# Optimization experiments

Hardware: AMD Instinct MI355X
Metric: run time of the kernel (lower is better)

Reference implementation:

```python
import jax, jax.numpy as jnp
import numpy as np

EPS = 1e-5
B, F, C, H, L, S = 8192, 128, 256, 512, 4, 10


def _gelu(x):
    return jax.nn.gelu(x, approximate=False)  # torch nn.GELU default = exact erf


def _ln(x, g, b):
    m = jnp.mean(x, axis=-1, keepdims=True)
    v = jnp.var(x, axis=-1, keepdims=True)  # biased, matches torch LayerNorm
    return (x - m) / jnp.sqrt(v + EPS) * g + b


def setup_inputs() -> dict:
    key = jax.random.key(0)
    ks = iter(jax.random.split(key, 40))

    def w(shape, fan_in):
        return jax.random.normal(next(ks), shape, jnp.float32) / np.float32(np.sqrt(fan_in))

    def z0(*s):
        return jnp.zeros(s, jnp.float32)

    return dict(
        x=jax.random.normal(next(ks), (B, F), jnp.float32),
        context=jax.random.normal(next(ks), (B, C), jnp.float32),
        u=jax.random.normal(next(ks), (S, B, F), jnp.float32),
        Wi=w((F, H), F), bi=z0(H),
        Wt1=w((1, H), 1), bt1=z0(H), Wt2=w((H, H), H), bt2=z0(H),
        Wc1=w((C, 2 * H), C), bc1=z0(2 * H), Wc2=w((2 * H, H), 2 * H), bc2=z0(H),
        Wv=w((L, H, H), H), bv=z0(L, H), Woa=w((L, H, H), H), boa=z0(L, H),
        g1=jnp.ones((L, H), jnp.float32), be1=z0(L, H),
        Wm1=w((L, H, 4 * H), H), bm1=z0(L, 4 * H),
        Wm2=w((L, 4 * H, H), 4 * H), bm2=z0(L, H),
        g2=jnp.ones((L, H), jnp.float32), be2=z0(L, H),
        Wcv=w((L, H, H), H), bcv=z0(L, H), Wco=w((L, H, H), H), bco=z0(L, H),
        scale=0.5 * jnp.ones((L,), jnp.float32),
        Wp1=w((H, H), H), bp1=z0(H), Wp2=w((H, F), H), bp2=z0(F),
    )


def _forward(x, context, u, Wi, bi, Wt1, bt1, Wt2, bt2, Wc1, bc1, Wc2, bc2,
             Wv, bv, Woa, boa, g1, be1, Wm1, bm1, Wm2, bm2, g2, be2,
             Wcv, bcv, Wco, bco, scale, Wp1, bp1, Wp2, bp2):
    n_steps = u.shape[0]
    dt = 1.0 / n_steps
    nb = x.shape[0]
    nl = Wv.shape[0]

    # context projection, computed once as in torch
    ctx = _gelu(context @ Wc1 + bc1) @ Wc2 + bc2  # [B,H]
    # seq_len==1 cross-attention: softmax over a single key == 1, so the output
    # is out_proj(v_proj(ctx)) and does not depend on x -> precompute per layer.
    vctx = jnp.einsum('bh,lhk->lbk', ctx, Wcv) + bcv[:, None, :]    # [L,B,H]
    xatt = jnp.einsum('lbh,lhk->lbk', vctx, Wco) + bco[:, None, :]  # [L,B,H]

    def vel(z, t):
        tt = jnp.clip(t, 0.0, 1.0)[:, None]                          # [B,1]
        h = z @ Wi + bi + (_gelu(tt @ Wt1 + bt1) @ Wt2 + bt2)        # [B,H]
        for l in range(nl):
            # seq_len==1 self-attention collapses to out_proj(v_proj(h))
            attn = (h @ Wv[l] + bv[l]) @ Woa[l] + boa[l]
            h = _ln(h + attn, g1[l], be1[l])
            mlp = _gelu(h @ Wm1[l] + bm1[l]) @ Wm2[l] + bm2[l]
            h = _ln(h + mlp, g2[l], be2[l])
            h = h + scale[l] * xatt[l]
        return _gelu(h @ Wp1 + bp1) @ Wp2 + bp2                      # [B,F]

    def step(carry, inp):
        z, ld = carry
        t_val, u_k = inp
        t = jnp.full((nb,), t_val, jnp.float32)
        zs = jax.lax.stop_gradient(z)  # matches z.detach()/leaf z_req in torch
        v, Ju = jax.jvp(lambda zz: vel(zz, t), (zs,), (u_k,))
        ld = ld + jnp.sum(u_k * Ju, axis=-1) * dt  # Hutchinson u^T J u
        return (zs + v * dt, ld), None

    ts = jnp.arange(n_steps, dtype=jnp.float32) * dt
    (z, log_det), _ = jax.lax.scan(step, (x, jnp.zeros((nb,), jnp.float32)), (ts, u))
    return z, log_det


def reference(x, context, u, Wi, bi, Wt1, bt1, Wt2, bt2, Wc1, bc1, Wc2, bc2,
              Wv, bv, Woa, boa, g1, be1, Wm1, bm1, Wm2, bm2, g2, be2,
              Wcv, bcv, Wco, bco, scale, Wp1, bp1, Wp2, bp2):
    return _forward(x, context, u, Wi, bi, Wt1, bt1, Wt2, bt2, Wc1, bc1, Wc2, bc2,
                    Wv, bv, Woa, boa, g1, be1, Wm1, bm1, Wm2, bm2, g2, be2,
                    Wcv, bcv, Wco, bco, scale, Wp1, bp1, Wp2, bp2)
```

## Files before the change

kernel.cpp:

```cpp
#include <hip/hip_runtime.h>
#include <math.h>

using floatx16 = __attribute__((ext_vector_type(16))) float;
using bf16x8   = __attribute__((ext_vector_type(8))) __bf16;
using ushort8  = __attribute__((ext_vector_type(8))) unsigned short;

__device__ __forceinline__ float b2f(unsigned short u) {
  unsigned v = ((unsigned)u) << 16; float f; __builtin_memcpy(&f, &v, 4); return f;
}
__device__ __forceinline__ unsigned short f2b(float f) {
  unsigned u; __builtin_memcpy(&u, &f, 4);
  u += 0x7fffu + ((u >> 16) & 1u);
  return (unsigned short)(u >> 16);
}
__device__ __forceinline__ float gelu_f(float x) {
  return 0.5f * x * (1.0f + erff(x * 0.7071067811865475f));
}
__device__ __forceinline__ float wred(float v) {
  #pragma unroll
  for (int off = 32; off > 0; off >>= 1) v += __shfl_xor(v, off, 64);
  return v;
}
__device__ __forceinline__ floatx16 zero16() {
  floatx16 z;
  #pragma unroll
  for (int e = 0; e < 16; e++) z[e] = 0.f;
  return z;
}

#define SWZS(r, c) (((r) << 5) + ((((c) ^ ((r) & 3))) << 3))

template<int MODE>
__global__ __launch_bounds__(256) void gemm_bt_k(
    const unsigned short* __restrict__ A, const unsigned short* __restrict__ Bt,
    void* __restrict__ C, const float* __restrict__ bias,
    const float* __restrict__ bias2, int M, int N, int K)
{
  __shared__ unsigned short As[128 * 32];
  __shared__ unsigned short Bs[128 * 32];
  const int tid  = threadIdx.x;
  const int lane = tid & 63;
  const int wave = tid >> 6;

  int bx = blockIdx.x, by = blockIdx.y;
  if ((gridDim.y & 7) == 0) {
    int lin = by * gridDim.x + bx;
    int xcd = lin & 7;
    int w   = lin >> 3;
    by = xcd * (gridDim.y >> 3) + w / gridDim.x;
    bx = w % gridDim.x;
  }
  const int row0 = by * 128;
  const int col0 = bx * 128;

  const int r0 = lane >> 2;
  const int cj = lane & 3;
  const unsigned short* Ag = A  + (size_t)(row0 + wave * 32 + r0) * K + cj * 8;
  const unsigned short* Bg = Bt + (size_t)(col0 + wave * 32 + r0) * K + cj * 8;
  unsigned short* Asw = &As[SWZS(wave * 32 + r0, cj)];
  unsigned short* Bsw = &Bs[SWZS(wave * 32 + r0, cj)];

  const int wr = wave >> 1, wc = wave & 1;
  const int m32 = lane & 31;
  const int hi  = lane >> 5;

  floatx16 acc[2][2];
  acc[0][0] = zero16(); acc[0][1] = zero16();
  acc[1][0] = zero16(); acc[1][1] = zero16();

  ushort8 ra0, ra1, rb0, rb1;
  ra0 = *(const ushort8*)(Ag);
  ra1 = *(const ushort8*)(Ag + (size_t)16 * K);
  rb0 = *(const ushort8*)(Bg);
  rb1 = *(const ushort8*)(Bg + (size_t)16 * K);

  for (int k0 = 0; k0 < K; k0 += 32) {
    __syncthreads();
    *(ushort8*)(Asw)             = ra0;
    *(ushort8*)(Asw + 16 * 32)   = ra1;
    *(ushort8*)(Bsw)             = rb0;
    *(ushort8*)(Bsw + 16 * 32)   = rb1;
    __syncthreads();
    if (k0 + 32 < K) {
      ra0 = *(const ushort8*)(Ag + k0 + 32);
      ra1 = *(const ushort8*)(Ag + (size_t)16 * K + k0 + 32);
      rb0 = *(const ushort8*)(Bg + k0 + 32);
      rb1 = *(const ushort8*)(Bg + (size_t)16 * K + k0 + 32);
    }
    bf16x8 af[2][2], bfr[2][2];
    #pragma unroll
    for (int i = 0; i < 2; i++)
      #pragma unroll
      for (int h = 0; h < 2; h++)
        af[i][h] = *(const bf16x8*)&As[SWZS(wr * 64 + i * 32 + m32, 2 * h + hi)];
    #pragma unroll
    for (int j = 0; j < 2; j++)
      #pragma unroll
      for (int h = 0; h < 2; h++)
        bfr[j][h] = *(const bf16x8*)&Bs[SWZS(wc * 64 + j * 32 + m32, 2 * h + hi)];
    #pragma unroll
    for (int h = 0; h < 2; h++)
      #pragma unroll
      for (int i = 0; i < 2; i++)
        #pragma unroll
        for (int j = 0; j < 2; j++)
          acc[i][j] = __builtin_amdgcn_mfma_f32_32x32x16_bf16(af[i][h], bfr[j][h], acc[i][j], 0, 0, 0);
  }

  #pragma unroll
  for (int j = 0; j < 2; j++) {
    int col = col0 + wc * 64 + j * 32 + m32;
    float bb = bias ? bias[col] : 0.f;
    if (MODE >= 2) { if (bias2) bb += bias2[col]; }
    #pragma unroll
    for (int i = 0; i < 2; i++) {
      int rb = row0 + wr * 64 + i * 32 + 4 * hi;
      if (MODE == 3) {
        #pragma unroll
        for (int pr = 0; pr < 8; pr++) {
          int re = rb + 2 * (pr & 1) + 8 * (pr >> 1);
          float p = acc[i][j][2 * pr] + bb;
          float t = acc[i][j][2 * pr + 1];
          float cdf = 0.5f * (1.0f + erff(p * 0.7071067811865475f));
          float pdf = 0.3989422804014327f * expf(-0.5f * p * p);
          ((unsigned short*)C)[(size_t)re * N + col]       = f2b(p * cdf);
          ((unsigned short*)C)[(size_t)(re + 1) * N + col] = f2b((cdf + p * pdf) * t);
        }
      } else {
        #pragma unroll
        for (int reg = 0; reg < 16; reg++) {
          int row = rb + (reg & 3) + 8 * (reg >> 2);
          float v = acc[i][j][reg];
          if (MODE == 0 || MODE == 1) v += bb;
          if (MODE == 2) { if ((reg & 1) == 0) v += bb; }
          if (MODE == 1) v = gelu_f(v);
          ((unsigned short*)C)[(size_t)row * N + col] = f2b(v);
        }
      }
    }
  }
}

__global__ __launch_bounds__(256) void gemm_vout_k(
    const unsigned short* __restrict__ A, const unsigned short* __restrict__ Bt,
    const float* __restrict__ bias, const float* __restrict__ u_cur,
    const float* __restrict__ u_next, float* __restrict__ zf,
    float* __restrict__ ldb, unsigned short* __restrict__ Abuf,
    int K, float dtv)
{
  constexpr int N = 128;
  __shared__ unsigned short As[128 * 32];
  __shared__ unsigned short Bs[128 * 32];
  __shared__ float red[64][2];
  const int tid = threadIdx.x, lane = tid & 63, wave = tid >> 6;
  const int row0 = blockIdx.x * 128;

  const int r0 = lane >> 2;
  const int cj = lane & 3;
  const unsigned short* Ag = A  + (size_t)(row0 + wave * 32 + r0) * K + cj * 8;
  const unsigned short* Bg = Bt + (size_t)(wave * 32 + r0) * K + cj * 8;
  unsigned short* Asw = &As[SWZS(wave * 32 + r0, cj)];
  unsigned short* Bsw = &Bs[SWZS(wave * 32 + r0, cj)];

  const int wr = wave >> 1, wc = wave & 1;
  const int m32 = lane & 31;
  const int hi  = lane >> 5;

  floatx16 acc[2][2];
  acc[0][0] = zero16(); acc[0][1] = zero16();
  acc[1][0] = zero16(); acc[1][1] = zero16();

  ushort8 ra0, ra1, rb0, rb1;
  ra0 = *(const ushort8*)(Ag);
  ra1 = *(const ushort8*)(Ag + (size_t)16 * K);
  rb0 = *(const ushort8*)(Bg);
  rb1 = *(const ushort8*)(Bg + (size_t)16 * K);

  for (int k0 = 0; k0 < K; k0 += 32) {
    __syncthreads();
    *(ushort8*)(Asw)           = ra0;
    *(ushort8*)(Asw + 16 * 32) = ra1;
    *(ushort8*)(Bsw)           = rb0;
    *(ushort8*)(Bsw + 16 * 32) = rb1;
    __syncthreads();
    if (k0 + 32 < K) {
      ra0 = *(const ushort8*)(Ag + k0 + 32);
      ra1 = *(const ushort8*)(Ag + (size_t)16 * K + k0 + 32);
      rb0 = *(const ushort8*)(Bg + k0 + 32);
      rb1 = *(const ushort8*)(Bg + (size_t)16 * K + k0 + 32);
    }
    bf16x8 af[2][2], bfr[2][2];
    #pragma unroll
    for (int i = 0; i < 2; i++)
      #pragma unroll
      for (int h = 0; h < 2; h++)
        af[i][h] = *(const bf16x8*)&As[SWZS(wr * 64 + i * 32 + m32, 2 * h + hi)];
    #pragma unroll
    for (int j = 0; j < 2; j++)
      #pragma unroll
      for (int h = 0; h < 2; h++)
        bfr[j][h] = *(const bf16x8*)&Bs[SWZS(wc * 64 + j * 32 + m32, 2 * h + hi)];
    #pragma unroll
    for (int h = 0; h < 2; h++)
      #pragma unroll
      for (int i = 0; i < 2; i++)
        #pragma unroll
        for (int j = 0; j < 2; j++)
          acc[i][j] = __builtin_amdgcn_mfma_f32_32x32x16_bf16(af[i][h], bfr[j][h], acc[i][j], 0, 0, 0);
  }

  #pragma unroll
  for (int i = 0; i < 2; i++) {
    #pragma unroll
    for (int pr = 0; pr < 8; pr++) {
      int re_loc = wr * 64 + i * 32 + 4 * hi + 2 * (pr & 1) + 8 * (pr >> 1);
      size_t growe = (size_t)(row0 + re_loc);
      size_t b = growe >> 1;
      float dacc = 0.f;
      #pragma unroll
      for (int j = 0; j < 2; j++) {
        int col = wc * 64 + j * 32 + m32;
        float v  = acc[i][j][2 * pr] + bias[col];
        float Ju = acc[i][j][2 * pr + 1];
        float z = zf[b * N + col] + v * dtv;
        zf[b * N + col] = z;
        Abuf[growe * N + col] = f2b(z);
        if (u_next) Abuf[(growe + 1) * N + col] = f2b(u_next[b * N + col]);
        dacc += u_cur[b * N + col] * Ju;
      }
      #pragma unroll
      for (int off = 1; off <= 16; off <<= 1) dacc += __shfl_xor(dacc, off, 64);
      if (m32 == 0) red[re_loc >> 1][wc] = dacc;
    }
  }
  __syncthreads();
  if (tid < 64) ldb[(row0 >> 1) + tid] += (red[tid][0] + red[tid][1]) * dtv;
}

__global__ __launch_bounds__(256) void ln_jvp_k(
    unsigned short* h, const unsigned short* __restrict__ r,
    const float* __restrict__ g, const float* __restrict__ be,
    const unsigned short* __restrict__ xatt, const float* __restrict__ sc_p,
    int Bhalf, int H)
{
  int gw = (int)((blockIdx.x * blockDim.x + threadIdx.x) >> 6);
  int lane = threadIdx.x & 63;
  if (gw >= Bhalf) return;
  int c0 = lane * 8;
  size_t op = (size_t)(2 * gw) * H + c0;
  size_t ot = op + H;
  ushort8 hp = *(const ushort8*)&h[op];
  ushort8 ht = *(const ushort8*)&h[ot];
  ushort8 rp = *(const ushort8*)&r[op];
  ushort8 rt = *(const ushort8*)&r[ot];
  float xv[8], dv[8];
  float s1 = 0.f, s2 = 0.f, sd = 0.f;
  #pragma unroll
  for (int j = 0; j < 8; j++) {
    xv[j] = b2f(hp[j]) + b2f(rp[j]);
    dv[j] = b2f(ht[j]) + b2f(rt[j]);
    s1 += xv[j]; s2 += xv[j] * xv[j]; sd += dv[j];
  }
  s1 = wred(s1); s2 = wred(s2); sd = wred(sd);
  float inv = 1.0f / (float)H;
  float m = s1 * inv;
  float var = s2 * inv - m * m;
  float rstd = rsqrtf(var + 1e-5f);
  float dm = sd * inv;
  float c = 0.f;
  #pragma unroll
  for (int j = 0; j < 8; j++) c += (xv[j] - m) * dv[j];
  c = wred(c);
  float cm = c * inv * rstd;
  float sl = sc_p ? *sc_p : 0.f;
  ushort8 oy, od;
  #pragma unroll
  for (int j = 0; j < 8; j++) {
    float xh = (xv[j] - m) * rstd;
    float gg = g[c0 + j];
    float y = xh * gg + be[c0 + j];
    if (xatt) y += sl * b2f(xatt[(size_t)gw * H + c0 + j]);
    float dy = gg * rstd * (dv[j] - dm - xh * cm);
    oy[j] = f2b(y); od[j] = f2b(dy);
  }
  *(ushort8*)&h[op] = oy;
  *(ushort8*)&h[ot] = od;
}

__global__ void transpose_cast_k(const float* __restrict__ W,
                                 unsigned short* __restrict__ Wt, int K, int N)
{
  __shared__ float tile[32][33];
  size_t off = (size_t)blockIdx.z * K * N;
  const float* Wp = W + off;
  unsigned short* Wtp = Wt + off;
  int bx = blockIdx.x, by = blockIdx.y;
  int tx = threadIdx.x, ty = threadIdx.y;
  #pragma unroll
  for (int i = ty; i < 32; i += 8)
    tile[i][tx] = Wp[(size_t)(by * 32 + i) * N + bx * 32 + tx];
  __syncthreads();
  #pragma unroll
  for (int i = ty; i < 32; i += 8)
    Wtp[(size_t)(bx * 32 + i) * K + by * 32 + tx] = f2b(tile[tx][i]);
}

__global__ __launch_bounds__(256) void zero_k(float* __restrict__ p, int n) {
  int i = (int)(blockIdx.x * blockDim.x + threadIdx.x);
  if (i < n) p[i] = 0.f;
}

__global__ __launch_bounds__(256) void combine_bias_k(
    const float* __restrict__ bvp, const float* __restrict__ Wb,
    const float* __restrict__ bo, float* __restrict__ bout, int H)
{
  int out = blockIdx.x * blockDim.x + threadIdx.x;
  int l   = blockIdx.y;
  int kc  = blockIdx.z;
  const float* A2 = Wb + (size_t)l * H * H;
  float s = (kc == 0) ? bo[(size_t)l * H + out] : 0.f;
  int kend = (kc + 1) * 64;
  for (int k = kc * 64; k < kend; k++) s += bvp[(size_t)l * H + k] * A2[(size_t)k * H + out];
  atomicAdd(&bout[(size_t)l * H + out], s);
}

__global__ __launch_bounds__(256) void cast_k(const float* __restrict__ in,
                                              unsigned short* __restrict__ out, size_t n) {
  size_t i = blockIdx.x * blockDim.x + threadIdx.x;
  if (i < n) out[i] = f2b(in[i]);
}

__global__ __launch_bounds__(512) void temb_all_k(
    const float* __restrict__ Wt1, const float* __restrict__ bt1,
    const float* __restrict__ Wt2, const float* __restrict__ bt2,
    float dtv, float* __restrict__ tvecs, int H)
{
  __shared__ float e[512];
  int j = threadIdx.x;
  float t = fminf(fmaxf((float)blockIdx.x * dtv, 0.f), 1.f);
  e[j] = gelu_f(t * Wt1[j] + bt1[j]);
  __syncthreads();
  float s = bt2[j];
  for (int k = 0; k < H; k++) s += e[k] * Wt2[(size_t)k * H + j];
  tvecs[(size_t)blockIdx.x * H + j] = s;
}

__global__ __launch_bounds__(256) void init_k(
    const float* __restrict__ x, const float* __restrict__ u0,
    float* __restrict__ zf, float* __restrict__ ld,
    unsigned short* __restrict__ Abuf, int BF, int Bsz, int F)
{
  int i = (int)(blockIdx.x * blockDim.x + threadIdx.x);
  if (i < BF) {
    int r = i / F, c = i - r * F;
    float v = x[i];
    zf[i] = v;
    Abuf[(size_t)(2 * r) * F + c]     = f2b(v);
    Abuf[(size_t)(2 * r + 1) * F + c] = f2b(u0[i]);
  }
  if (i < Bsz) ld[i] = 0.f;
}

__global__ __launch_bounds__(256) void final_k(
    const float* __restrict__ zf, const float* __restrict__ ld,
    float* __restrict__ out, int BF, int Bsz)
{
  int i = (int)(blockIdx.x * blockDim.x + threadIdx.x);
  if (i < BF) out[i] = zf[i];
  if (i < Bsz) out[BF + i] = ld[i];
}

extern "C" void kernel_launch(void* const* d_in, const int* in_sizes, int n_in,
                              void* d_out, int out_size, void* d_ws, size_t ws_size,
                              hipStream_t stream) {
  constexpr int B = 8192, F = 128, C = 256, H = 512, L = 4, S = 10;
  constexpr int B2 = 2 * B;
  constexpr int BF = B * F;
  const float dtv = 1.0f / S;

  const float* x    = (const float*)d_in[0];
  const float* ctxI = (const float*)d_in[1];
  const float* u    = (const float*)d_in[2];
  const float* Wi   = (const float*)d_in[3];
  const float* bi   = (const float*)d_in[4];
  const float* Wt1  = (const float*)d_in[5];
  const float* bt1  = (const float*)d_in[6];
  const float* Wt2  = (const float*)d_in[7];
  const float* bt2  = (const float*)d_in[8];
  const float* Wc1  = (const float*)d_in[9];
  const float* bc1  = (const float*)d_in[10];
  const float* Wc2  = (const float*)d_in[11];
  const float* bc2  = (const float*)d_in[12];
  const float* Wv   = (const float*)d_in[13];
  const float* bv   = (const float*)d_in[14];
  const float* Woa  = (const float*)d_in[15];
  const float* boa  = (const float*)d_in[16];
  const float* g1   = (const float*)d_in[17];
  const float* be1  = (const float*)d_in[18];
  const float* Wm1  = (const float*)d_in[19];
  const float* bm1  = (const float*)d_in[20];
  const float* Wm2  = (const float*)d_in[21];
  const float* bm2  = (const float*)d_in[22];
  const float* g2   = (const float*)d_in[23];
  const float* be2  = (const float*)d_in[24];
  const float* Wcv  = (const float*)d_in[25];
  const float* bcv  = (const float*)d_in[26];
  const float* Wco  = (const float*)d_in[27];
  const float* bco  = (const float*)d_in[28];
  const float* scal = (const float*)d_in[29];
  const float* Wp1  = (const float*)d_in[30];
  const float* bp1  = (const float*)d_in[31];
  const float* Wp2  = (const float*)d_in[32];
  const float* bp2  = (const float*)d_in[33];

  char* wp = (char*)d_ws;
  auto alloc = [&](size_t bytes) -> void* {
    void* r = (void*)wp;
    wp += (bytes + 255) & ~(size_t)255;
    return r;
  };
  unsigned short* wWit  = (unsigned short*)alloc((size_t)H * F * 2);
  unsigned short* wWc1t = (unsigned short*)alloc((size_t)2 * H * C * 2);
  unsigned short* wWc2t = (unsigned short*)alloc((size_t)H * 2 * H * 2);
  unsigned short* wWvoT = (unsigned short*)alloc((size_t)L * H * H * 2);
  unsigned short* wCtxT = (unsigned short*)alloc((size_t)L * H * H * 2);
  unsigned short* wWm1t = (unsigned short*)alloc((size_t)L * 4 * H * H * 2);
  unsigned short* wWm2t = (unsigned short*)alloc((size_t)L * H * 4 * H * 2);
  unsigned short* wWp1t = (unsigned short*)alloc((size_t)H * H * 2);
  unsigned short* wWp2t = (unsigned short*)alloc((size_t)F * H * 2);
  unsigned short* wOaT  = (unsigned short*)alloc((size_t)L * H * H * 2);
  unsigned short* wCoT  = (unsigned short*)alloc((size_t)L * H * H * 2);
  unsigned short* wVb   = (unsigned short*)alloc((size_t)L * H * H * 2);
  unsigned short* wCvb  = (unsigned short*)alloc((size_t)L * H * H * 2);
  float* bcomb          = (float*)alloc((size_t)2 * L * H * 4);
  float* bvo  = bcomb;
  float* cbvo = bcomb + (size_t)L * H;
  float* tvecs          = (float*)alloc((size_t)S * H * 4);
  unsigned short* ctxc  = (unsigned short*)alloc((size_t)B * C * 2);
  unsigned short* Abuf  = (unsigned short*)alloc((size_t)B2 * F * 2);
  unsigned short* hbuf  = (unsigned short*)alloc((size_t)B2 * H * 2);
  unsigned short* tmp2  = (unsigned short*)alloc((size_t)B2 * H * 2);
  unsigned short* mbuf  = (unsigned short*)alloc((size_t)B2 * 4 * H * 2);
  unsigned short* xattb = (unsigned short*)alloc((size_t)L * B * H * 2);
  float* zf             = (float*)alloc((size_t)B * F * 4);
  float* ldb            = (float*)alloc((size_t)B * 4);
  (void)ws_size; (void)in_sizes; (void)n_in; (void)out_size;

  auto T = [&](const float* W, unsigned short* Wt, int K, int N, int Lz) {
    dim3 g(N / 32, K / 32, Lz);
    transpose_cast_k<<<g, dim3(32, 8), 0, stream>>>(W, Wt, K, N);
  };
  auto G = [&](int mode, const unsigned short* A, const unsigned short* Bt, void* Cc,
               const float* bias, const float* bias2, int M, int N, int K) {
    dim3 g(N / 128, M / 128);
    switch (mode) {
      case 0: gemm_bt_k<0><<<g, 256, 0, stream>>>(A, Bt, Cc, bias, bias2, M, N, K); break;
      case 1: gemm_bt_k<1><<<g, 256, 0, stream>>>(A, Bt, Cc, bias, bias2, M, N, K); break;
      case 2: gemm_bt_k<2><<<g, 256, 0, stream>>>(A, Bt, Cc, bias, bias2, M, N, K); break;
      case 3: gemm_bt_k<3><<<g, 256, 0, stream>>>(A, Bt, Cc, bias, bias2, M, N, K); break;
    }
  };

  T(Wi,  wWit,  F, H, 1);
  T(Wc1, wWc1t, C, 2 * H, 1);
  T(Wc2, wWc2t, 2 * H, H, 1);
  T(Wm1, wWm1t, H, 4 * H, L);
  T(Wm2, wWm2t, 4 * H, H, L);
  T(Wp1, wWp1t, H, H, 1);
  T(Wp2, wWp2t, H, F, 1);
  T(Woa, wOaT, H, H, L);
  T(Wco, wCoT, H, H, L);
  cast_k<<<((size_t)L * H * H + 255) / 256, 256, 0, stream>>>(Wv,  wVb,  (size_t)L * H * H);
  cast_k<<<((size_t)L * H * H + 255) / 256, 256, 0, stream>>>(Wcv, wCvb, (size_t)L * H * H);
  for (int l = 0; l < L; l++) {
    size_t o2 = (size_t)l * H * H;
    G(0, wOaT + o2, wVb  + o2, wWvoT + o2, nullptr, nullptr, H, H, H);
    G(0, wCoT + o2, wCvb + o2, wCtxT + o2, nullptr, nullptr, H, H, H);
  }
  zero_k<<<(2 * L * H + 255) / 256, 256, 0, stream>>>(bcomb, 2 * L * H);
  combine_bias_k<<<dim3(H / 256, L, H / 64), 256, 0, stream>>>(bv,  Woa, boa, bvo,  H);
  combine_bias_k<<<dim3(H / 256, L, H / 64), 256, 0, stream>>>(bcv, Wco, bco, cbvo, H);

  cast_k<<<(B * C + 255) / 256, 256, 0, stream>>>(ctxI, ctxc, (size_t)B * C);
  G(1, ctxc, wWc1t, mbuf, bc1, nullptr, B, 2 * H, C);
  G(0, mbuf, wWc2t, tmp2, bc2, nullptr, B, H, 2 * H);
  for (int l = 0; l < L; l++)
    G(0, tmp2, wCtxT + (size_t)l * H * H, xattb + (size_t)l * B * H,
      cbvo + l * H, nullptr, B, H, H);

  temb_all_k<<<S, H, 0, stream>>>(Wt1, bt1, Wt2, bt2, dtv, tvecs, H);
  init_k<<<(BF + 255) / 256, 256, 0, stream>>>(x, u, zf, ldb, Abuf, BF, B, F);

  for (int s = 0; s < S; s++) {
    G(2, Abuf, wWit, hbuf, bi, tvecs + (size_t)s * H, B2, H, F);
    for (int l = 0; l < L; l++) {
      size_t o2 = (size_t)l * H * H;
      size_t om = (size_t)l * 4 * H * H;
      G(2, hbuf, wWvoT + o2, tmp2, bvo + l * H, nullptr, B2, H, H);
      ln_jvp_k<<<B / 4, 256, 0, stream>>>(hbuf, tmp2, g1 + l * H, be1 + l * H,
                                          nullptr, nullptr, B, H);
      G(3, hbuf, wWm1t + om, mbuf, bm1 + (size_t)l * 4 * H, nullptr, B2, 4 * H, H);
      G(2, mbuf, wWm2t + om, tmp2, bm2 + l * H, nullptr, B2, H, 4 * H);
      ln_jvp_k<<<B / 4, 256, 0, stream>>>(hbuf, tmp2, g2 + l * H, be2 + l * H,
                                          xattb + (size_t)l * B * H, scal + l, B, H);
    }
    G(3, hbuf, wWp1t, tmp2, bp1, nullptr, B2, H, H);
    const float* u_cur = u + (size_t)s * BF;
    const float* u_next = (s + 1 < S) ? u + (size_t)(s + 1) * BF : nullptr;
    gemm_vout_k<<<B2 / 128, 256, 0, stream>>>(
        tmp2, wWp2t, bp2, u_cur, u_next, zf, ldb, Abuf, H, dtv);
  }

  final_k<<<(BF + 255) / 256, 256, 0, stream>>>(zf, ldb, (float*)d_out, BF, B);
}
```

Before: 8.646 ms.

## Double-buffer LDS in GEMM kernels and add wide-tile kernel for MLP up-projection

Switches the shared-memory tiles of the GEMM kernels to ping-pong double buffers, which removes one __syncthreads per K-step because the next tile is written into the other buffer. Adds a 128x256-tile GEMM with a GELU-JVP epilogue, used for the MLP first layer (N=4H), so each A tile is reused across twice as many columns. The cost is more LDS and more accumulator registers per block, which may lower occupancy.

Result: faster. 8.459 ms (-2.2%).

```diff
diff --git a/kernel.cpp b/kernel.cpp
--- a/kernel.cpp
+++ b/kernel.cpp
@@ -36,8 +36,8 @@
     void* __restrict__ C, const float* __restrict__ bias,
     const float* __restrict__ bias2, int M, int N, int K)
 {
-  __shared__ unsigned short As[128 * 32];
-  __shared__ unsigned short Bs[128 * 32];
+  __shared__ unsigned short As[2 * 128 * 32];
+  __shared__ unsigned short Bs[2 * 128 * 32];
   const int tid  = threadIdx.x;
   const int lane = tid & 63;
   const int wave = tid >> 6;
@@ -57,8 +57,7 @@
   const int cj = lane & 3;
   const unsigned short* Ag = A  + (size_t)(row0 + wave * 32 + r0) * K + cj * 8;
   const unsigned short* Bg = Bt + (size_t)(col0 + wave * 32 + r0) * K + cj * 8;
-  unsigned short* Asw = &As[SWZS(wave * 32 + r0, cj)];
-  unsigned short* Bsw = &Bs[SWZS(wave * 32 + r0, cj)];
+  const int aw0 = SWZS(wave * 32 + r0, cj);
 
   const int wr = wave >> 1, wc = wave & 1;
   const int m32 = lane & 31;
@@ -74,12 +73,14 @@
   rb0 = *(const ushort8*)(Bg);
   rb1 = *(const ushort8*)(Bg + (size_t)16 * K);
 
+  int p = 0;
   for (int k0 = 0; k0 < K; k0 += 32) {
-    __syncthreads();
-    *(ushort8*)(Asw)             = ra0;
-    *(ushort8*)(Asw + 16 * 32)   = ra1;
-    *(ushort8*)(Bsw)             = rb0;
-    *(ushort8*)(Bsw + 16 * 32)   = rb1;
+    unsigned short* Ab = &As[p * 4096];
+    unsigned short* Bb = &Bs[p * 4096];
+    *(ushort8*)(Ab + aw0)            = ra0;
+    *(ushort8*)(Ab + aw0 + 16 * 32)  = ra1;
+    *(ushort8*)(Bb + aw0)            = rb0;
+    *(ushort8*)(Bb + aw0 + 16 * 32)  = rb1;
     __syncthreads();
     if (k0 + 32 < K) {
       ra0 = *(const ushort8*)(Ag + k0 + 32);
@@ -92,12 +93,12 @@
     for (int i = 0; i < 2; i++)
       #pragma unroll
       for (int h = 0; h < 2; h++)
-        af[i][h] = *(const bf16x8*)&As[SWZS(wr * 64 + i * 32 + m32, 2 * h + hi)];
+        af[i][h] = *(const bf16x8*)&Ab[SWZS(wr * 64 + i * 32 + m32, 2 * h + hi)];
     #pragma unroll
     for (int j = 0; j < 2; j++)
       #pragma unroll
       for (int h = 0; h < 2; h++)
-        bfr[j][h] = *(const bf16x8*)&Bs[SWZS(wc * 64 + j * 32 + m32, 2 * h + hi)];
+        bfr[j][h] = *(const bf16x8*)&Bb[SWZS(wc * 64 + j * 32 + m32, 2 * h + hi)];
     #pragma unroll
     for (int h = 0; h < 2; h++)
       #pragma unroll
@@ -105,6 +106,7 @@
         #pragma unroll
         for (int j = 0; j < 2; j++)
           acc[i][j] = __builtin_amdgcn_mfma_f32_32x32x16_bf16(af[i][h], bfr[j][h], acc[i][j], 0, 0, 0);
+    p ^= 1;
   }
 
   #pragma unroll
@@ -119,12 +121,12 @@
         #pragma unroll
         for (int pr = 0; pr < 8; pr++) {
           int re = rb + 2 * (pr & 1) + 8 * (pr >> 1);
-          float p = acc[i][j][2 * pr] + bb;
-          float t = acc[i][j][2 * pr + 1];
-          float cdf = 0.5f * (1.0f + erff(p * 0.7071067811865475f));
-          float pdf = 0.3989422804014327f * expf(-0.5f * p * p);
-          ((unsigned short*)C)[(size_t)re * N + col]       = f2b(p * cdf);
-          ((unsigned short*)C)[(size_t)(re + 1) * N + col] = f2b((cdf + p * pdf) * t);
+          float pv = acc[i][j][2 * pr] + bb;
+          float tv = acc[i][j][2 * pr + 1];
+          float cdf = 0.5f * (1.0f + erff(pv * 0.7071067811865475f));
+          float pdf = 0.3989422804014327f * expf(-0.5f * pv * pv);
+          ((unsigned short*)C)[(size_t)re * N + col]       = f2b(pv * cdf);
+          ((unsigned short*)C)[(size_t)(re + 1) * N + col] = f2b((cdf + pv * pdf) * tv);
         }
       } else {
         #pragma unroll
@@ -141,6 +143,111 @@
   }
 }
 
+__global__ __launch_bounds__(256, 2) void gemm_wide3_k(
+    const unsigned short* __restrict__ A, const unsigned short* __restrict__ Bt,
+    unsigned short* __restrict__ C, const float* __restrict__ bias,
+    int M, int N, int K)
+{
+  __shared__ unsigned short As[2 * 128 * 32];
+  __shared__ unsigned short Bs[2 * 256 * 32];
+  const int tid  = threadIdx.x;
+  const int lane = tid & 63;
+  const int wave = tid >> 6;
+
+  int bx = blockIdx.x, by = blockIdx.y;
+  if ((gridDim.y & 7) == 0) {
+    int lin = by * gridDim.x + bx;
+    int xcd = lin & 7;
+    int w   = lin >> 3;
+    by = xcd * (gridDim.y >> 3) + w / gridDim.x;
+    bx = w % gridDim.x;
+  }
+  const int row0 = by * 128;
+  const int col0 = bx * 256;
+
+  const int r0 = lane >> 2;
+  const int cj = lane & 3;
+  const unsigned short* Ag = A  + (size_t)(row0 + wave * 32 + r0) * K + cj * 8;
+  const unsigned short* Bg = Bt + (size_t)(col0 + wave * 64 + r0) * K + cj * 8;
+  const int awr = wave * 32 + r0;
+  const int bwr = wave * 64 + r0;
+
+  const int wr = wave >> 1, wc = wave & 1;
+  const int m32 = lane & 31;
+  const int hi  = lane >> 5;
+
+  floatx16 acc[2][4];
+  #pragma unroll
+  for (int i = 0; i < 2; i++)
+    #pragma unroll
+    for (int j = 0; j < 4; j++) acc[i][j] = zero16();
+
+  ushort8 ra0, ra1, rbv[4];
+  ra0 = *(const ushort8*)(Ag);
+  ra1 = *(const ushort8*)(Ag + (size_t)16 * K);
+  #pragma unroll
+  for (int t = 0; t < 4; t++)
+    rbv[t] = *(const ushort8*)(Bg + (size_t)16 * t * K);
+
+  int p = 0;
+  for (int k0 = 0; k0 < K; k0 += 32) {
+    unsigned short* Ab = &As[p * 4096];
+    unsigned short* Bb = &Bs[p * 8192];
+    *(ushort8*)&Ab[SWZS(awr, cj)]      = ra0;
+    *(ushort8*)&Ab[SWZS(awr + 16, cj)] = ra1;
+    #pragma unroll
+    for (int t = 0; t < 4; t++)
+      *(ushort8*)&Bb[SWZS(bwr + 16 * t, cj)] = rbv[t];
+    __syncthreads();
+    if (k0 + 32 < K) {
+      ra0 = *(const ushort8*)(Ag + k0 + 32);
+      ra1 = *(const ushort8*)(Ag + (size_t)16 * K + k0 + 32);
+      #pragma unroll
+      for (int t = 0; t < 4; t++)
+        rbv[t] = *(const ushort8*)(Bg + (size_t)16 * t * K + k0 + 32);
+    }
+    bf16x8 af[2][2], bfr[4][2];
+    #pragma unroll
+    for (int i = 0; i < 2; i++)
+      #pragma unroll
+      for (int h = 0; h < 2; h++)
+        af[i][h] = *(const bf16x8*)&Ab[SWZS(wr * 64 + i * 32 + m32, 2 * h + hi)];
+    #pragma unroll
+    for (int j = 0; j < 4; j++)
+      #pragma unroll
+      for (int h = 0; h < 2; h++)
+        bfr[j][h] = *(const bf16x8*)&Bb[SWZS(wc * 128 + j * 32 + m32, 2 * h + hi)];
+    #pragma unroll
+    for (int h = 0; h < 2; h++)
+      #pragma unroll
+      for (int i = 0; i < 2; i++)
+        #pragma unroll
+        for (int j = 0; j < 4; j++)
+          acc[i][j] = __builtin_amdgcn_mfma_f32_32x32x16_bf16(af[i][h], bfr[j][h], acc[i][j], 0, 0, 0);
+    p ^= 1;
+  }
+
+  #pragma unroll
+  for (int j = 0; j < 4; j++) {
+    int col = col0 + wc * 128 + j * 32 + m32;
+    float bb = bias[col];
+    #pragma unroll
+    for (int i = 0; i < 2; i++) {
+      int rb = row0 + wr * 64 + i * 32 + 4 * hi;
+      #pragma unroll
+      for (int pr = 0; pr < 8; pr++) {
+        int re = rb + 2 * (pr & 1) + 8 * (pr >> 1);
+        float pv = acc[i][j][2 * pr] + bb;
+        float tv = acc[i][j][2 * pr + 1];
+        float cdf = 0.5f * (1.0f + erff(pv * 0.7071067811865475f));
+        float pdf = 0.3989422804014327f * expf(-0.5f * pv * pv);
+        C[(size_t)re * N + col]       = f2b(pv * cdf);
+        C[(size_t)(re + 1) * N + col] = f2b((cdf + pv * pdf) * tv);
+      }
+    }
+  }
+}
+
 __global__ __launch_bounds__(256) void gemm_vout_k(
     const unsigned short* __restrict__ A, const unsigned short* __restrict__ Bt,
     const float* __restrict__ bias, const float* __restrict__ u_cur,
@@ -149,8 +256,8 @@
     int K, float dtv)
 {
   constexpr int N = 128;
-  __shared__ unsigned short As[128 * 32];
-  __shared__ unsigned short Bs[128 * 32];
+  __shared__ unsigned short As[2 * 128 * 32];
+  __shared__ unsigned short Bs[2 * 128 * 32];
   __shared__ float red[64][2];
   const int tid = threadIdx.x, lane = tid & 63, wave = tid >> 6;
   const int row0 = blockIdx.x * 128;
@@ -159,8 +266,7 @@
   const int cj = lane & 3;
   const unsigned short* Ag = A  + (size_t)(row0 + wave * 32 + r0) * K + cj * 8;
   const unsigned short* Bg = Bt + (size_t)(wave * 32 + r0) * K + cj * 8;
-  unsigned short* Asw = &As[SWZS(wave * 32 + r0, cj)];
-  unsigned short* Bsw = &Bs[SWZS(wave * 32 + r0, cj)];
+  const int aw0 = SWZS(wave * 32 + r0, cj);
 
   const int wr = wave >> 1, wc = wave & 1;
   const int m32 = lane & 31;
@@ -176,12 +282,14 @@
   rb0 = *(const ushort8*)(Bg);
   rb1 = *(const ushort8*)(Bg + (size_t)16 * K);
 
+  int p = 0;
   for (int k0 = 0; k0 < K; k0 += 32) {
-    __syncthreads();
-    *(ushort8*)(Asw)           = ra0;
-    *(ushort8*)(Asw + 16 * 32) = ra1;
-    *(ushort8*)(Bsw)           = rb0;
-    *(ushort8*)(Bsw + 16 * 32) = rb1;
+    unsigned short* Ab = &As[p * 4096];
+    unsigned short* Bb = &Bs[p * 4096];
+    *(ushort8*)(Ab + aw0)           = ra0;
+    *(ushort8*)(Ab + aw0 + 16 * 32) = ra1;
+    *(ushort8*)(Bb + aw0)           = rb0;
+    *(ushort8*)(Bb + aw0 + 16 * 32) = rb1;
     __syncthreads();
     if (k0 + 32 < K) {
       ra0 = *(const ushort8*)(Ag + k0 + 32);
@@ -194,12 +302,12 @@
     for (int i = 0; i < 2; i++)
       #pragma unroll
       for (int h = 0; h < 2; h++)
-        af[i][h] = *(const bf16x8*)&As[SWZS(wr * 64 + i * 32 + m32, 2 * h + hi)];
+        af[i][h] = *(const bf16x8*)&Ab[SWZS(wr * 64 + i * 32 + m32, 2 * h + hi)];
     #pragma unroll
     for (int j = 0; j < 2; j++)
       #pragma unroll
       for (int h = 0; h < 2; h++)
-        bfr[j][h] = *(const bf16x8*)&Bs[SWZS(wc * 64 + j * 32 + m32, 2 * h + hi)];
+        bfr[j][h] = *(const bf16x8*)&Bb[SWZS(wc * 64 + j * 32 + m32, 2 * h + hi)];
     #pragma unroll
     for (int h = 0; h < 2; h++)
       #pragma unroll
@@ -207,6 +315,7 @@
         #pragma unroll
         for (int j = 0; j < 2; j++)
           acc[i][j] = __builtin_amdgcn_mfma_f32_32x32x16_bf16(af[i][h], bfr[j][h], acc[i][j], 0, 0, 0);
+    p ^= 1;
   }
 
   #pragma unroll
@@ -499,7 +608,8 @@
       G(2, hbuf, wWvoT + o2, tmp2, bvo + l * H, nullptr, B2, H, H);
       ln_jvp_k<<<B / 4, 256, 0, stream>>>(hbuf, tmp2, g1 + l * H, be1 + l * H,
                                           nullptr, nullptr, B, H);
-      G(3, hbuf, wWm1t + om, mbuf, bm1 + (size_t)l * 4 * H, nullptr, B2, 4 * H, H);
+      gemm_wide3_k<<<dim3(4 * H / 256, B2 / 128), 256, 0, stream>>>(
+          hbuf, wWm1t + om, mbuf, bm1 + (size_t)l * 4 * H, B2, 4 * H, H);
       G(2, mbuf, wWm2t + om, tmp2, bm2 + l * H, nullptr, B2, H, 4 * H);
       ln_jvp_k<<<B / 4, 256, 0, stream>>>(hbuf, tmp2, g2 + l * H, be2 + l * H,
                                           xattb + (size_t)l * B * H, scal + l, B, H);
```
